# Optimization experiments

Hardware: AMD Instinct MI355X
Metric: run time of the kernel (lower is better)

The kernel has to match this reference:

```python
import jax, jax.numpy as jnp
import numpy as np

B, LD, LM, D, H = 2, 2048, 2048, 1024, 16
DH = D // H  # attention head size = 64


def setup_inputs() -> dict:
    key = jax.random.key(0)
    ks = jax.random.split(key, 9)
    s = 1.0 / np.sqrt(D)
    return {
        "hidden_states": jax.random.normal(ks[0], (B, LD, D), jnp.float32),
        "encoder_hidden_states": jax.random.normal(ks[1], (B, LM, D), jnp.float32),
        "attention_mask": jax.random.randint(ks[2], (B, LM), 0, 2, jnp.int32),
        "head_mask": jnp.zeros((B, LD), jnp.int32),
        "Wq": jax.random.normal(ks[3], (D, D), jnp.float32) * s,
        "bq": jax.random.normal(ks[4], (D,), jnp.float32) * 0.01,
        "Wk": jax.random.normal(ks[5], (D, D), jnp.float32) * s,
        "bk": jax.random.normal(ks[6], (D,), jnp.float32) * 0.01,
        "Wv": jax.random.normal(ks[7], (D, D), jnp.float32) * s,
        "bv": jax.random.normal(ks[8], (D,), jnp.float32) * 0.01,
    }


def reference(hidden_states, encoder_hidden_states, attention_mask, head_mask,
              Wq, bq, Wk, bk, Wv, bv):
    # torch Linear: y = x @ W.T + b, W is [out, in]
    def split_heads(x, L):
        return x.reshape(x.shape[0], L, H, DH).transpose(0, 2, 1, 3)  # [B,H,L,DH]

    q = split_heads(hidden_states @ Wq.T + bq, LD)
    k = split_heads(encoder_hidden_states @ Wk.T + bk, LM)
    v = split_heads(encoder_hidden_states @ Wv.T + bv, LM)

    scores = jnp.einsum("bhqd,bhkd->bhqk", q, k) / jnp.sqrt(jnp.float32(DH))
    add_mask = -1e30 * (1.0 - attention_mask.astype(scores.dtype))  # [B, Lm]
    scores = scores + add_mask[:, None, None, :]
    probs = jax.nn.softmax(scores, axis=-1)
    # dropout prob 0 (eval) -> identity
    hmask = 1.0 - head_mask.astype(probs.dtype)  # [B, Ld]
    probs = probs * hmask[:, None, :, None]
    ctx = jnp.einsum("bhqk,bhkd->bhqd", probs, v)  # [B,H,Ld,DH]
    return ctx.transpose(0, 2, 1, 3).reshape(ctx.shape[0], LD, D)
```

## Files before the change

kernel.cpp:

```cpp
#include <hip/hip_runtime.h>
#include <math.h>

typedef _Float16 half_t;
typedef _Float16 halfx8 __attribute__((ext_vector_type(8)));
typedef _Float16 halfx4 __attribute__((ext_vector_type(4)));
typedef float floatx4 __attribute__((ext_vector_type(4)));
typedef float floatx16 __attribute__((ext_vector_type(16)));
typedef unsigned int uintx2 __attribute__((ext_vector_type(2)));
typedef unsigned int uintx4 __attribute__((ext_vector_type(4)));

typedef __attribute__((address_space(3))) void lds_t;
typedef const __attribute__((address_space(1))) void gmem_t;

static constexpr int kB = 2;
static constexpr int kLD = 2048;
static constexpr int kLM = 2048;
static constexpr int kD = 1024;
static constexpr int kH = 16;
static constexpr int kDH = 64;

__device__ __forceinline__ float exp2_fast(float x) {
#if __has_builtin(__builtin_amdgcn_exp2f)
  return __builtin_amdgcn_exp2f(x);
#else
  return exp2f(x);
#endif
}

__global__ __launch_bounds__(256) void convert_all(
    const float* __restrict__ s0, const float* __restrict__ s1,
    const float* __restrict__ s2, const float* __restrict__ s3,
    const float* __restrict__ s4, const int* __restrict__ am,
    half_t* __restrict__ d0, half_t* __restrict__ d1,
    half_t* __restrict__ d2, half_t* __restrict__ d3, half_t* __restrict__ d4,
    float* __restrict__ maskf)
{
  const size_t N0 = (size_t)kB * kLD * kD;
  const size_t N1 = N0 + (size_t)kB * kLM * kD;
  const size_t N2 = N1 + (size_t)kD * kD;
  const size_t N3 = N2 + (size_t)kD * kD;
  const size_t N4 = N3 + (size_t)kD * kD;
  const size_t N5 = N4 + (size_t)kB * kLM;
  size_t idx = ((size_t)blockIdx.x * blockDim.x + threadIdx.x) * 4;
  if (idx >= N5) return;
  if (idx >= N4) {
    const size_t off = idx - N4;
    int4 m = *(const int4*)(am + off);
    float4 o;
    o.x = m.x ? 0.0f : -1e30f;
    o.y = m.y ? 0.0f : -1e30f;
    o.z = m.z ? 0.0f : -1e30f;
    o.w = m.w ? 0.0f : -1e30f;
    *(float4*)(maskf + off) = o;
    return;
  }
  const float* s; half_t* d; size_t off;
  if (idx < N0)      { s = s0; d = d0; off = idx; }
  else if (idx < N1) { s = s1; d = d1; off = idx - N0; }
  else if (idx < N2) { s = s2; d = d2; off = idx - N1; }
  else if (idx < N3) { s = s3; d = d3; off = idx - N2; }
  else               { s = s4; d = d4; off = idx - N3; }
  float4 v = *(const float4*)(s + off);
  halfx4 hv;
  hv[0] = (half_t)v.x; hv[1] = (half_t)v.y; hv[2] = (half_t)v.z; hv[3] = (half_t)v.w;
  *(halfx4*)(d + off) = hv;
}

__global__ __launch_bounds__(256, 2) void qkv_gemm(
    const half_t* __restrict__ xdec, const half_t* __restrict__ xenc,
    const half_t* __restrict__ wq, const half_t* __restrict__ wk,
    const half_t* __restrict__ wv,
    const float* __restrict__ bq, const float* __restrict__ bk,
    const float* __restrict__ bv,
    half_t* __restrict__ qbuf, half_t* __restrict__ kbuf,
    half_t* __restrict__ vtbuf)
{
  const int mode = blockIdx.z;
  const half_t* Ag = (mode == 0) ? xdec : xenc;
  const half_t* Bg = (mode == 0) ? wq : (mode == 1) ? wk : wv;
  const float* bias = (mode == 0) ? bq : (mode == 1) ? bk : bv;

  __shared__ alignas(16) half_t Alds[128 * 64];
  __shared__ alignas(16) half_t Blds[128 * 64];

  const int m0 = blockIdx.x * 128;
  const int n0 = blockIdx.y * 128;
  const int tid = threadIdx.x;
  const int lane = tid & 63;
  const int wid = tid >> 6;
  const int wr = wid >> 1, wc = wid & 1;
  const int l15 = lane & 15, lhi = lane >> 4;

  floatx4 acc[4][4] = {};

  for (int k0 = 0; k0 < kD; k0 += 64) {
    __syncthreads();
#pragma unroll
    for (int i = 0; i < 4; ++i) {
      const int ob = wid * 4096 + i * 1024;
      const int lo = ob + lane * 16;
      const int row = lo >> 7;
      const int colh = (lo & 127) >> 1;
      const half_t* ga = Ag + (size_t)(m0 + row) * kD + k0 + colh;
      const half_t* gb = Bg + (size_t)(n0 + row) * kD + k0 + colh;
      __builtin_amdgcn_global_load_lds((gmem_t*)ga, (lds_t*)((char*)Alds + ob), 16, 0, 0);
      __builtin_amdgcn_global_load_lds((gmem_t*)gb, (lds_t*)((char*)Blds + ob), 16, 0, 0);
    }
    __syncthreads();

#pragma unroll
    for (int ks = 0; ks < 2; ++ks) {
      halfx8 af[4], bf[4];
#pragma unroll
      for (int mt = 0; mt < 4; ++mt)
        af[mt] = *(const halfx8*)(Alds + (wr * 64 + mt * 16 + l15) * 64 + ks * 32 + lhi * 8);
#pragma unroll
      for (int nt = 0; nt < 4; ++nt)
        bf[nt] = *(const halfx8*)(Blds + (wc * 64 + nt * 16 + l15) * 64 + ks * 32 + lhi * 8);
#pragma unroll
      for (int mt = 0; mt < 4; ++mt)
#pragma unroll
        for (int nt = 0; nt < 4; ++nt)
          acc[mt][nt] = __builtin_amdgcn_mfma_f32_16x16x32_f16(af[mt], bf[nt], acc[mt][nt], 0, 0, 0);
    }
  }

#pragma unroll
  for (int nt = 0; nt < 4; ++nt) {
    const int n = n0 + wc * 64 + nt * 16 + l15;
    const float bb = bias[n];
    const int h = n >> 6, dv = n & 63;
#pragma unroll
    for (int mt = 0; mt < 4; ++mt) {
#pragma unroll
      for (int r = 0; r < 4; ++r) {
        const int m = m0 + wr * 64 + mt * 16 + lhi * 4 + r;
        const int b = m >> 11, rowl = m & 2047;
        float v = acc[mt][nt][r] + bb;
        if (mode == 0) {
          v *= 0.18033688011112042f;
          qbuf[((size_t)(b * kH + h) * kLD + rowl) * kDH + dv] = (half_t)v;
        } else if (mode == 1) {
          kbuf[((size_t)(b * kH + h) * kLM + rowl) * kDH + dv] = (half_t)v;
        } else {
          vtbuf[((size_t)(b * kH + h) * kDH + dv) * kLM + rowl] = (half_t)v;
        }
      }
    }
  }
}

__global__ __launch_bounds__(256) void attn_kernel(
    const half_t* __restrict__ qbuf, const half_t* __restrict__ kbuf,
    const half_t* __restrict__ vtbuf, const float* __restrict__ maskf,
    const int* __restrict__ hmask, float* __restrict__ out)
{
  const int x = blockIdx.x;
  const int ordered = (x & 7) * 128 + (x >> 3);
  const int bh = ordered >> 5, qt = ordered & 31;
  const int b = bh >> 4, h = bh & 15;

  const int tid = threadIdx.x;
  const int lane = tid & 63;
  const int wid = tid >> 6;
  const int p = wid >> 1;
  const int w = wid & 1;
  const int ql = lane & 31;
  const int hi = lane >> 5;

  __shared__ alignas(16) char smem[33 * 1024];
  half_t* Klds = (half_t*)(smem + p * 16384);
  half_t* Vlds = (half_t*)(smem + p * 16384 + 8192);
  float* mlds = (float*)(smem + 32768);

  const half_t* kbase = kbuf + (size_t)bh * (kLM * kDH) + (size_t)p * 1024 * kDH;
  const half_t* vtbase = vtbuf + (size_t)bh * (kDH * kLM) + p * 1024;
  const float* mbase = maskf + b * kLM + p * 1024;

  const int lrow = lane >> 3;
  const int lchunk = lane & 7;
  const int xcol = (lchunk ^ lrow) * 8;
  const size_t koff = (size_t)(w * 32 + lrow) * kDH + xcol;
  const size_t voff = (size_t)(w * 32 + lrow) * kLM + xcol;

  const int qg = qt * 64 + w * 32 + ql;
  halfx8 qf[4];
#pragma unroll
  for (int ks = 0; ks < 4; ++ks)
    qf[ks] = *(const halfx8*)(qbuf + ((size_t)bh * kLD + qg) * kDH + ks * 16 + hi * 8);

  floatx16 ctx0 = {}, ctx1 = {};
  float m_run = -1e30f, l_run = 0.0f;

#pragma unroll 1
  for (int t = 0; t < 16; ++t) {
    const int kv0 = t * 64;
    __syncthreads();
#pragma unroll
    for (int i = 0; i < 4; ++i) {
      __builtin_amdgcn_global_load_lds(
          (gmem_t*)(kbase + (size_t)kv0 * kDH + koff + i * 8 * kDH),
          (lds_t*)((char*)Klds + w * 4096 + i * 1024), 16, 0, 0);
      __builtin_amdgcn_global_load_lds(
          (gmem_t*)(vtbase + kv0 + voff + (size_t)i * 8 * kLM),
          (lds_t*)((char*)Vlds + w * 4096 + i * 1024), 16, 0, 0);
    }
    __syncthreads();

    floatx16 S0, S1;
#pragma unroll
    for (int g = 0; g < 4; ++g) {
      float4 a0 = *(const float4*)(mbase + kv0 + g * 8 + hi * 4);
      float4 a1 = *(const float4*)(mbase + kv0 + 32 + g * 8 + hi * 4);
      S0[g * 4 + 0] = a0.x; S0[g * 4 + 1] = a0.y; S0[g * 4 + 2] = a0.z; S0[g * 4 + 3] = a0.w;
      S1[g * 4 + 0] = a1.x; S1[g * 4 + 1] = a1.y; S1[g * 4 + 2] = a1.z; S1[g * 4 + 3] = a1.w;
    }

#pragma unroll
    for (int ks = 0; ks < 4; ++ks) {
      const int off0 = (ql * 128 + ks * 32 + hi * 16) ^ ((ql & 7) << 4);
      halfx8 kf0 = *(const halfx8*)((const char*)Klds + off0);
      S0 = __builtin_amdgcn_mfma_f32_32x32x16_f16(kf0, qf[ks], S0, 0, 0, 0);
      const int off1 = ((32 + ql) * 128 + ks * 32 + hi * 16) ^ ((ql & 7) << 4);
      halfx8 kf1 = *(const halfx8*)((const char*)Klds + off1);
      S1 = __builtin_amdgcn_mfma_f32_32x32x16_f16(kf1, qf[ks], S1, 0, 0, 0);
    }

    float mx8[8];
#pragma unroll
    for (int i = 0; i < 8; ++i)
      mx8[i] = fmaxf(fmaxf(S0[i], S0[i + 8]), fmaxf(S1[i], S1[i + 8]));
#pragma unroll
    for (int i = 0; i < 4; ++i) mx8[i] = fmaxf(mx8[i], mx8[i + 4]);
    float mx = fmaxf(fmaxf(mx8[0], mx8[1]), fmaxf(mx8[2], mx8[3]));
    mx = fmaxf(mx, __shfl_xor(mx, 32));

    if (!__all(mx <= m_run + 8.0f)) {
      const float mn = fmaxf(m_run, mx);
      const float sc = exp2_fast(m_run - mn);
      m_run = mn;
      l_run *= sc;
#pragma unroll
      for (int i = 0; i < 16; ++i) { ctx0[i] *= sc; ctx1[i] *= sc; }
    }

#pragma unroll
    for (int i = 0; i < 16; ++i) {
      S0[i] = exp2_fast(S0[i] - m_run);
      S1[i] = exp2_fast(S1[i] - m_run);
    }
    float sm8[8];
#pragma unroll
    for (int i = 0; i < 8; ++i)
      sm8[i] = (S0[i] + S0[i + 8]) + (S1[i] + S1[i + 8]);
#pragma unroll
    for (int i = 0; i < 4; ++i) sm8[i] += sm8[i + 4];
    float ps = (sm8[0] + sm8[1]) + (sm8[2] + sm8[3]);
    ps += __shfl_xor(ps, 32);
    l_run += ps;

    halfx8 pb[4];
#pragma unroll
    for (int sl = 0; sl < 4; ++sl) {
      const floatx16& P = (sl < 2) ? S0 : S1;
      const int rA = (sl & 1) * 8;
      unsigned wa = __builtin_bit_cast(unsigned, __builtin_amdgcn_cvt_pkrtz(P[rA + 0], P[rA + 1]));
      unsigned wb = __builtin_bit_cast(unsigned, __builtin_amdgcn_cvt_pkrtz(P[rA + 2], P[rA + 3]));
      unsigned wc = __builtin_bit_cast(unsigned, __builtin_amdgcn_cvt_pkrtz(P[rA + 4], P[rA + 5]));
      unsigned wd = __builtin_bit_cast(unsigned, __builtin_amdgcn_cvt_pkrtz(P[rA + 6], P[rA + 7]));
      uintx2 u1 = __builtin_amdgcn_permlane32_swap(wa, wc, false, false);
      uintx2 u2 = __builtin_amdgcn_permlane32_swap(wb, wd, false, false);
      uintx4 u;
      u[0] = u1[0]; u[1] = u2[0]; u[2] = u1[1]; u[3] = u2[1];
      pb[sl] = __builtin_bit_cast(halfx8, u);
    }

#pragma unroll
    for (int sl = 0; sl < 4; ++sl) {
      const int off0 = (ql * 128 + sl * 32 + hi * 16) ^ ((ql & 7) << 4);
      halfx8 vf0 = *(const halfx8*)((const char*)Vlds + off0);
      ctx0 = __builtin_amdgcn_mfma_f32_32x32x16_f16(vf0, pb[sl], ctx0, 0, 0, 0);
      const int off1 = ((32 + ql) * 128 + sl * 32 + hi * 16) ^ ((ql & 7) << 4);
      halfx8 vf1 = *(const halfx8*)((const char*)Vlds + off1);
      ctx1 = __builtin_amdgcn_mfma_f32_32x32x16_f16(vf1, pb[sl], ctx1, 0, 0, 0);
    }
  }

  __syncthreads();
  {
    float* Op = (float*)(smem + p * 16384);
    const int q_local = w * 32 + ql;
#pragma unroll
    for (int g = 0; g < 4; ++g) {
#pragma unroll
      for (int pr = 0; pr < 2; ++pr) {
        const int r = g * 4 + pr * 2;
        const int dv0 = pr * 2 + 8 * g + 4 * hi;
        const int off0 = (q_local * 256 + dv0 * 4) ^ ((q_local & 7) << 4);
        *(float2*)((char*)Op + off0) = make_float2(ctx0[r], ctx0[r + 1]);
        const int off1 = (q_local * 256 + (dv0 + 32) * 4) ^ ((q_local & 7) << 4);
        *(float2*)((char*)Op + off1) = make_float2(ctx1[r], ctx1[r + 1]);
      }
    }
    if (hi == 0) {
      mlds[p * 128 + q_local] = m_run;
      mlds[p * 128 + 64 + q_local] = l_run;
    }
  }
  __syncthreads();

#pragma unroll
  for (int it = 0; it < 4; ++it) {
    const int idx = it * 256 + tid;
    const int q = idx >> 4, c4 = idx & 15;
    const int off = (q * 256 + c4 * 16) ^ ((q & 7) << 4);
    float4 o0 = *(const float4*)(smem + off);
    float4 o1 = *(const float4*)(smem + 16384 + off);
    const float m0 = mlds[q], l0 = mlds[64 + q];
    const float m1 = mlds[128 + q], l1 = mlds[192 + q];
    const float mm = fmaxf(m0, m1);
    float w0 = exp2_fast(m0 - mm), w1 = exp2_fast(m1 - mm);
    const int qglob = qt * 64 + q;
    const float inv = (hmask[b * kLD + qglob] ? 0.0f : 1.0f) / (l0 * w0 + l1 * w1);
    w0 *= inv; w1 *= inv;
    float4 o;
    o.x = o0.x * w0 + o1.x * w1;
    o.y = o0.y * w0 + o1.y * w1;
    o.z = o0.z * w0 + o1.z * w1;
    o.w = o0.w * w0 + o1.w * w1;
    *(float4*)(out + (((size_t)(b * kLD + qglob)) << 10) + h * 64 + c4 * 4) = o;
  }
}

extern "C" void kernel_launch(void* const* d_in, const int* in_sizes, int n_in,
                              void* d_out, int out_size, void* d_ws, size_t ws_size,
                              hipStream_t stream)
{
  const float* hs   = (const float*)d_in[0];
  const float* ehs  = (const float*)d_in[1];
  const int*   am   = (const int*)d_in[2];
  const int*   hm   = (const int*)d_in[3];
  const float* Wq   = (const float*)d_in[4];
  const float* bq   = (const float*)d_in[5];
  const float* Wk   = (const float*)d_in[6];
  const float* bk   = (const float*)d_in[7];
  const float* Wv   = (const float*)d_in[8];
  const float* bv   = (const float*)d_in[9];
  float* out = (float*)d_out;

  char* ws = (char*)d_ws;
  half_t* xdec_h = (half_t*)(ws);
  half_t* xenc_h = (half_t*)(ws + (8ull << 20));
  half_t* wq_h   = (half_t*)(ws + (16ull << 20));
  half_t* wk_h   = (half_t*)(ws + (18ull << 20));
  half_t* wv_h   = (half_t*)(ws + (20ull << 20));
  half_t* q_buf  = (half_t*)(ws + (22ull << 20));
  half_t* k_buf  = (half_t*)(ws + (30ull << 20));
  half_t* vt_buf = (half_t*)(ws + (38ull << 20));
  float*  maskf  = (float*)(ws + (46ull << 20));

  convert_all<<<11268, 256, 0, stream>>>(hs, ehs, Wq, Wk, Wv, am,
                                         xdec_h, xenc_h, wq_h, wk_h, wv_h, maskf);
  qkv_gemm<<<dim3(32, 8, 3), 256, 0, stream>>>(xdec_h, xenc_h, wq_h, wk_h, wv_h,
                                               bq, bk, bv, q_buf, k_buf, vt_buf);
  attn_kernel<<<1024, 256, 0, stream>>>(q_buf, k_buf, vt_buf, maskf, hm, out);
}
```

Before: 213.2 us.

## Double-buffer K/V tiles in attention, pack mask to bits, transpose V GEMM epilogue

The attention loop now works on 32-key tiles with two LDS buffers, so the global-to-LDS load of the next tile is issued before the current tile is computed and only one barrier is needed per iteration. The additive float mask is replaced by a packed 32-bit mask word per 32 keys. That word is applied by AND-ing the exponentials with sign-extracted bits instead of preloading -1e30 into the score accumulator. The V projection swaps the MFMA operands so its transposed stores run along contiguous sequence positions, which is meant to coalesce the vtbuf writes. In exchange there are twice as many loop iterations with smaller MFMA batches, plus a serial 32-load bit-packing step in the conversion kernel.

```diff
diff --git a/kernel.cpp b/kernel.cpp
--- a/kernel.cpp
+++ b/kernel.cpp
@@ -27,31 +27,36 @@
 #endif
 }
 
+__device__ __forceinline__ int sbfe1(int src, int pos) {
+#if __has_builtin(__builtin_amdgcn_sbfe)
+  return __builtin_amdgcn_sbfe(src, pos, 1);
+#else
+  return ((int)((unsigned)src << (31 - pos))) >> 31;
+#endif
+}
+
 __global__ __launch_bounds__(256) void convert_all(
     const float* __restrict__ s0, const float* __restrict__ s1,
     const float* __restrict__ s2, const float* __restrict__ s3,
     const float* __restrict__ s4, const int* __restrict__ am,
     half_t* __restrict__ d0, half_t* __restrict__ d1,
     half_t* __restrict__ d2, half_t* __restrict__ d3, half_t* __restrict__ d4,
-    float* __restrict__ maskf)
+    unsigned int* __restrict__ maskbits)
 {
   const size_t N0 = (size_t)kB * kLD * kD;
   const size_t N1 = N0 + (size_t)kB * kLM * kD;
   const size_t N2 = N1 + (size_t)kD * kD;
   const size_t N3 = N2 + (size_t)kD * kD;
   const size_t N4 = N3 + (size_t)kD * kD;
-  const size_t N5 = N4 + (size_t)kB * kLM;
   size_t idx = ((size_t)blockIdx.x * blockDim.x + threadIdx.x) * 4;
-  if (idx >= N5) return;
   if (idx >= N4) {
-    const size_t off = idx - N4;
-    int4 m = *(const int4*)(am + off);
-    float4 o;
-    o.x = m.x ? 0.0f : -1e30f;
-    o.y = m.y ? 0.0f : -1e30f;
-    o.z = m.z ? 0.0f : -1e30f;
-    o.w = m.w ? 0.0f : -1e30f;
-    *(float4*)(maskf + off) = o;
+    const size_t wi = (idx - N4) >> 2;
+    if (wi >= (size_t)(kB * kLM / 32)) return;
+    const int* src = am + wi * 32;
+    unsigned int wbits = 0;
+#pragma unroll
+    for (int j = 0; j < 32; ++j) wbits |= (src[j] ? 1u : 0u) << j;
+    maskbits[wi] = wbits;
     return;
   }
   const float* s; half_t* d; size_t off;
@@ -117,32 +122,57 @@
 #pragma unroll
       for (int nt = 0; nt < 4; ++nt)
         bf[nt] = *(const halfx8*)(Blds + (wc * 64 + nt * 16 + l15) * 64 + ks * 32 + lhi * 8);
-#pragma unroll
-      for (int mt = 0; mt < 4; ++mt)
-#pragma unroll
-        for (int nt = 0; nt < 4; ++nt)
-          acc[mt][nt] = __builtin_amdgcn_mfma_f32_16x16x32_f16(af[mt], bf[nt], acc[mt][nt], 0, 0, 0);
-    }
-  }
-
-#pragma unroll
-  for (int nt = 0; nt < 4; ++nt) {
-    const int n = n0 + wc * 64 + nt * 16 + l15;
-    const float bb = bias[n];
-    const int h = n >> 6, dv = n & 63;
-#pragma unroll
-    for (int mt = 0; mt < 4; ++mt) {
-#pragma unroll
-      for (int r = 0; r < 4; ++r) {
-        const int m = m0 + wr * 64 + mt * 16 + lhi * 4 + r;
+      if (mode != 2) {
+#pragma unroll
+        for (int mt = 0; mt < 4; ++mt)
+#pragma unroll
+          for (int nt = 0; nt < 4; ++nt)
+            acc[mt][nt] = __builtin_amdgcn_mfma_f32_16x16x32_f16(af[mt], bf[nt], acc[mt][nt], 0, 0, 0);
+      } else {
+#pragma unroll
+        for (int mt = 0; mt < 4; ++mt)
+#pragma unroll
+          for (int nt = 0; nt < 4; ++nt)
+            acc[mt][nt] = __builtin_amdgcn_mfma_f32_16x16x32_f16(bf[nt], af[mt], acc[mt][nt], 0, 0, 0);
+      }
+    }
+  }
+
+  if (mode != 2) {
+#pragma unroll
+    for (int nt = 0; nt < 4; ++nt) {
+      const int n = n0 + wc * 64 + nt * 16 + l15;
+      const float bb = bias[n];
+      const int h = n >> 6, dv = n & 63;
+#pragma unroll
+      for (int mt = 0; mt < 4; ++mt) {
+#pragma unroll
+        for (int r = 0; r < 4; ++r) {
+          const int m = m0 + wr * 64 + mt * 16 + lhi * 4 + r;
+          const int b = m >> 11, rowl = m & 2047;
+          float v = acc[mt][nt][r] + bb;
+          if (mode == 0) {
+            v *= 0.18033688011112042f;
+            qbuf[((size_t)(b * kH + h) * kLD + rowl) * kDH + dv] = (half_t)v;
+          } else {
+            kbuf[((size_t)(b * kH + h) * kLM + rowl) * kDH + dv] = (half_t)v;
+          }
+        }
+      }
+    }
+  } else {
+#pragma unroll
+    for (int nt = 0; nt < 4; ++nt) {
+      const float4 bb4 = *(const float4*)(bias + n0 + wc * 64 + nt * 16 + lhi * 4);
+#pragma unroll
+      for (int mt = 0; mt < 4; ++mt) {
+        const int m = m0 + wr * 64 + mt * 16 + l15;
         const int b = m >> 11, rowl = m & 2047;
-        float v = acc[mt][nt][r] + bb;
-        if (mode == 0) {
-          v *= 0.18033688011112042f;
-          qbuf[((size_t)(b * kH + h) * kLD + rowl) * kDH + dv] = (half_t)v;
-        } else if (mode == 1) {
-          kbuf[((size_t)(b * kH + h) * kLM + rowl) * kDH + dv] = (half_t)v;
-        } else {
+#pragma unroll
+        for (int r = 0; r < 4; ++r) {
+          const int n = n0 + wc * 64 + nt * 16 + lhi * 4 + r;
+          const int h = n >> 6, dv = n & 63;
+          float v = acc[mt][nt][r] + ((const float*)&bb4)[r];
           vtbuf[((size_t)(b * kH + h) * kDH + dv) * kLM + rowl] = (half_t)v;
         }
       }
@@ -152,7 +182,7 @@
 
 __global__ __launch_bounds__(256) void attn_kernel(
     const half_t* __restrict__ qbuf, const half_t* __restrict__ kbuf,
-    const half_t* __restrict__ vtbuf, const float* __restrict__ maskf,
+    const half_t* __restrict__ vtbuf, const unsigned int* __restrict__ maskbits,
     const int* __restrict__ hmask, float* __restrict__ out)
 {
   const int x = blockIdx.x;
@@ -169,19 +199,30 @@
   const int hi = lane >> 5;
 
   __shared__ alignas(16) char smem[33 * 1024];
-  half_t* Klds = (half_t*)(smem + p * 16384);
-  half_t* Vlds = (half_t*)(smem + p * 16384 + 8192);
+  char* Kb = smem + p * 16384;
+  char* Vb = smem + p * 16384 + 8192;
   float* mlds = (float*)(smem + 32768);
 
   const half_t* kbase = kbuf + (size_t)bh * (kLM * kDH) + (size_t)p * 1024 * kDH;
   const half_t* vtbase = vtbuf + (size_t)bh * (kDH * kLM) + p * 1024;
-  const float* mbase = maskf + b * kLM + p * 1024;
-
-  const int lrow = lane >> 3;
-  const int lchunk = lane & 7;
-  const int xcol = (lchunk ^ lrow) * 8;
-  const size_t koff = (size_t)(w * 32 + lrow) * kDH + xcol;
-  const size_t voff = (size_t)(w * 32 + lrow) * kLM + xcol;
+  const unsigned int* mwptr = maskbits + b * 64 + p * 32;
+
+  const int kl_row = lane >> 3;
+  const int k_srcoff = ((lane & 7) ^ kl_row) * 8;
+  const int vl_row = lane >> 2;
+  const int v_srcoff = ((lane & 3) ^ (vl_row & 3)) * 8;
+
+  auto STAGE = [&](char* Kdst, char* Vdst, int kv0s) {
+#pragma unroll
+    for (int i = 0; i < 2; ++i) {
+      __builtin_amdgcn_global_load_lds(
+          (gmem_t*)(kbase + (size_t)(kv0s + w * 16 + i * 8 + kl_row) * kDH + k_srcoff),
+          (lds_t*)(Kdst + w * 2048 + i * 1024), 16, 0, 0);
+      __builtin_amdgcn_global_load_lds(
+          (gmem_t*)(vtbase + (size_t)(w * 32 + i * 16 + vl_row) * kLM + kv0s + v_srcoff),
+          (lds_t*)(Vdst + w * 2048 + i * 1024), 16, 0, 0);
+    }
+  };
 
   const int qg = qt * 64 + w * 32 + ql;
   halfx8 qf[4];
@@ -192,47 +233,33 @@
   floatx16 ctx0 = {}, ctx1 = {};
   float m_run = -1e30f, l_run = 0.0f;
 
+  STAGE(Kb, Vb, 0);
+  unsigned int maskw = mwptr[0];
+  __syncthreads();
+
 #pragma unroll 1
-  for (int t = 0; t < 16; ++t) {
-    const int kv0 = t * 64;
-    __syncthreads();
-#pragma unroll
-    for (int i = 0; i < 4; ++i) {
-      __builtin_amdgcn_global_load_lds(
-          (gmem_t*)(kbase + (size_t)kv0 * kDH + koff + i * 8 * kDH),
-          (lds_t*)((char*)Klds + w * 4096 + i * 1024), 16, 0, 0);
-      __builtin_amdgcn_global_load_lds(
-          (gmem_t*)(vtbase + kv0 + voff + (size_t)i * 8 * kLM),
-          (lds_t*)((char*)Vlds + w * 4096 + i * 1024), 16, 0, 0);
-    }
-    __syncthreads();
-
-    floatx16 S0, S1;
-#pragma unroll
-    for (int g = 0; g < 4; ++g) {
-      float4 a0 = *(const float4*)(mbase + kv0 + g * 8 + hi * 4);
-      float4 a1 = *(const float4*)(mbase + kv0 + 32 + g * 8 + hi * 4);
-      S0[g * 4 + 0] = a0.x; S0[g * 4 + 1] = a0.y; S0[g * 4 + 2] = a0.z; S0[g * 4 + 3] = a0.w;
-      S1[g * 4 + 0] = a1.x; S1[g * 4 + 1] = a1.y; S1[g * 4 + 2] = a1.z; S1[g * 4 + 3] = a1.w;
-    }
-
+  for (int t = 0; t < 32; ++t) {
+    const int kv0 = t * 32;
+    char* Kc = Kb + (t & 1) * 4096;
+    char* Vc = Vb + (t & 1) * 4096;
+    if (t < 31) STAGE(Kb + ((t & 1) ^ 1) * 4096, Vb + ((t & 1) ^ 1) * 4096, kv0 + 32);
+    const unsigned int mw = maskw;
+    if (t < 31) maskw = mwptr[t + 1];
+
+    floatx16 S = {};
 #pragma unroll
     for (int ks = 0; ks < 4; ++ks) {
-      const int off0 = (ql * 128 + ks * 32 + hi * 16) ^ ((ql & 7) << 4);
-      halfx8 kf0 = *(const halfx8*)((const char*)Klds + off0);
-      S0 = __builtin_amdgcn_mfma_f32_32x32x16_f16(kf0, qf[ks], S0, 0, 0, 0);
-      const int off1 = ((32 + ql) * 128 + ks * 32 + hi * 16) ^ ((ql & 7) << 4);
-      halfx8 kf1 = *(const halfx8*)((const char*)Klds + off1);
-      S1 = __builtin_amdgcn_mfma_f32_32x32x16_f16(kf1, qf[ks], S1, 0, 0, 0);
-    }
-
-    float mx8[8];
-#pragma unroll
-    for (int i = 0; i < 8; ++i)
-      mx8[i] = fmaxf(fmaxf(S0[i], S0[i + 8]), fmaxf(S1[i], S1[i + 8]));
-#pragma unroll
-    for (int i = 0; i < 4; ++i) mx8[i] = fmaxf(mx8[i], mx8[i + 4]);
-    float mx = fmaxf(fmaxf(mx8[0], mx8[1]), fmaxf(mx8[2], mx8[3]));
+      const int off = ql * 128 + ((ks * 32 + hi * 16) ^ ((ql & 7) << 4));
+      halfx8 kf = *(const halfx8*)(Kc + off);
+      S = __builtin_amdgcn_mfma_f32_32x32x16_f16(kf, qf[ks], S, 0, 0, 0);
+    }
+
+    float m8[8];
+#pragma unroll
+    for (int i = 0; i < 8; ++i) m8[i] = fmaxf(S[i], S[i + 8]);
+#pragma unroll
+    for (int i = 0; i < 4; ++i) m8[i] = fmaxf(m8[i], m8[i + 4]);
+    float mx = fmaxf(fmaxf(m8[0], m8[1]), fmaxf(m8[2], m8[3]));
     mx = fmaxf(mx, __shfl_xor(mx, 32));
 
     if (!__all(mx <= m_run + 8.0f)) {
@@ -244,30 +271,30 @@
       for (int i = 0; i < 16; ++i) { ctx0[i] *= sc; ctx1[i] *= sc; }
     }
 
+    const int vrot = (int)(mw >> (hi * 4));
 #pragma unroll
     for (int i = 0; i < 16; ++i) {
-      S0[i] = exp2_fast(S0[i] - m_run);
-      S1[i] = exp2_fast(S1[i] - m_run);
-    }
-    float sm8[8];
-#pragma unroll
-    for (int i = 0; i < 8; ++i)
-      sm8[i] = (S0[i] + S0[i + 8]) + (S1[i] + S1[i + 8]);
-#pragma unroll
-    for (int i = 0; i < 4; ++i) sm8[i] += sm8[i + 4];
-    float ps = (sm8[0] + sm8[1]) + (sm8[2] + sm8[3]);
+      float e = exp2_fast(S[i] - m_run);
+      const int mb = sbfe1(vrot, (i & 3) + 8 * (i >> 2));
+      S[i] = __builtin_bit_cast(float, __builtin_bit_cast(int, e) & mb);
+    }
+    float s8[8];
+#pragma unroll
+    for (int i = 0; i < 8; ++i) s8[i] = S[i] + S[i + 8];
+#pragma unroll
+    for (int i = 0; i < 4; ++i) s8[i] += s8[i + 4];
+    float ps = (s8[0] + s8[1]) + (s8[2] + s8[3]);
     ps += __shfl_xor(ps, 32);
     l_run += ps;
 
-    halfx8 pb[4];
-#pragma unroll
-    for (int sl = 0; sl < 4; ++sl) {
-      const floatx16& P = (sl < 2) ? S0 : S1;
-      const int rA = (sl & 1) * 8;
-      unsigned wa = __builtin_bit_cast(unsigned, __builtin_amdgcn_cvt_pkrtz(P[rA + 0], P[rA + 1]));
-      unsigned wb = __builtin_bit_cast(unsigned, __builtin_amdgcn_cvt_pkrtz(P[rA + 2], P[rA + 3]));
-      unsigned wc = __builtin_bit_cast(unsigned, __builtin_amdgcn_cvt_pkrtz(P[rA + 4], P[rA + 5]));
-      unsigned wd = __builtin_bit_cast(unsigned, __builtin_amdgcn_cvt_pkrtz(P[rA + 6], P[rA + 7]));
+    halfx8 pb[2];
+#pragma unroll
+    for (int sl = 0; sl < 2; ++sl) {
+      const int rA = sl * 8;
+      unsigned wa = __builtin_bit_cast(unsigned, __builtin_amdgcn_cvt_pkrtz(S[rA + 0], S[rA + 1]));
+      unsigned wb = __builtin_bit_cast(unsigned, __builtin_amdgcn_cvt_pkrtz(S[rA + 2], S[rA + 3]));
+      unsigned wc = __builtin_bit_cast(unsigned, __builtin_amdgcn_cvt_pkrtz(S[rA + 4], S[rA + 5]));
+      unsigned wd = __builtin_bit_cast(unsigned, __builtin_amdgcn_cvt_pkrtz(S[rA + 6], S[rA + 7]));
       uintx2 u1 = __builtin_amdgcn_permlane32_swap(wa, wc, false, false);
       uintx2 u2 = __builtin_amdgcn_permlane32_swap(wb, wd, false, false);
       uintx4 u;
@@ -276,17 +303,17 @@
     }
 
 #pragma unroll
-    for (int sl = 0; sl < 4; ++sl) {
-      const int off0 = (ql * 128 + sl * 32 + hi * 16) ^ ((ql & 7) << 4);
-      halfx8 vf0 = *(const halfx8*)((const char*)Vlds + off0);
+    for (int sl = 0; sl < 2; ++sl) {
+      const int chunk = ((sl * 2 + hi) << 4) ^ ((ql & 3) << 4);
+      halfx8 vf0 = *(const halfx8*)(Vc + ql * 64 + chunk);
       ctx0 = __builtin_amdgcn_mfma_f32_32x32x16_f16(vf0, pb[sl], ctx0, 0, 0, 0);
-      const int off1 = ((32 + ql) * 128 + sl * 32 + hi * 16) ^ ((ql & 7) << 4);
-      halfx8 vf1 = *(const halfx8*)((const char*)Vlds + off1);
+      halfx8 vf1 = *(const halfx8*)(Vc + (32 + ql) * 64 + chunk);
       ctx1 = __builtin_amdgcn_mfma_f32_32x32x16_f16(vf1, pb[sl], ctx1, 0, 0, 0);
     }
-  }
-
-  __syncthreads();
+
+    __syncthreads();
+  }
+
   {
     float* Op = (float*)(smem + p * 16384);
     const int q_local = w * 32 + ql;
@@ -357,11 +384,11 @@
   half_t* q_buf  = (half_t*)(ws + (22ull << 20));
   half_t* k_buf  = (half_t*)(ws + (30ull << 20));
   half_t* vt_buf = (half_t*)(ws + (38ull << 20));
-  float*  maskf  = (float*)(ws + (46ull << 20));
-
-  convert_all<<<11268, 256, 0, stream>>>(hs, ehs, Wq, Wk, Wv, am,
-                                         xdec_h, xenc_h, wq_h, wk_h, wv_h, maskf);
+  unsigned int* maskbits = (unsigned int*)(ws + (46ull << 20));
+
+  convert_all<<<11265, 256, 0, stream>>>(hs, ehs, Wq, Wk, Wv, am,
+                                         xdec_h, xenc_h, wq_h, wk_h, wv_h, maskbits);
   qkv_gemm<<<dim3(32, 8, 3), 256, 0, stream>>>(xdec_h, xenc_h, wq_h, wk_h, wv_h,
                                                bq, bk, bv, q_buf, k_buf, vt_buf);
-  attn_kernel<<<1024, 256, 0, stream>>>(q_buf, k_buf, vt_buf, maskf, hm, out);
-}
+  attn_kernel<<<1024, 256, 0, stream>>>(q_buf, k_buf, vt_buf, maskbits, hm, out);
+}
```

After: 220.1 us. 1.03x slower.
